# Kernel optimization log

Hardware: AMD Instinct MI355X
Metric: run time of the kernel (lower is better)

The kernel has to match this reference:

```python
import jax, jax.numpy as jnp
import numpy as np

NX = 768
N_HEAD = 12
R = 8
SCALING = 16.0  # lora_alpha*r / r = lora_alpha
NEG = 1e10


def setup_inputs() -> dict:
    key = jax.random.key(0)
    ks = jax.random.split(key, 7)
    B, S = 2, 2048
    return {
        "x": jax.random.normal(ks[0], (B, S, NX), dtype=jnp.float32),
        "w_attn": jax.random.normal(ks[1], (NX, 3 * NX), dtype=jnp.float32) * 0.02,
        "b_attn": jax.random.normal(ks[2], (3 * NX,), dtype=jnp.float32) * 0.02,
        "lora_A": jax.random.normal(ks[3], (3 * R, NX), dtype=jnp.float32) * 0.02,
        "lora_B": jax.random.normal(ks[4], (3 * NX, R), dtype=jnp.float32) * 0.02,
        "w_proj": jax.random.normal(ks[5], (NX, NX), dtype=jnp.float32) * 0.02,
        "b_proj": jax.random.normal(ks[6], (NX,), dtype=jnp.float32) * 0.02,
    }


def reference(x, w_attn, b_attn, lora_A, lora_B, w_proj, b_proj):
    B, S, _ = x.shape
    dh = NX // N_HEAD

    # --- LoRA-augmented QKV projection (MergedLinear, fan_in_fan_out=True, unmerged) ---
    qkv = x @ w_attn + b_attn  # [B,S,3*NX]
    A = lora_A.reshape(3, R, NX)          # per-chunk A_i: [r, nx]
    Bm = lora_B.reshape(3, NX, R)         # per-chunk B_i: [nx, r]
    # x @ (B_i @ A_i).T = (x @ A_i.T) @ B_i.T, grouped over q/k/v chunks c
    t = jnp.einsum('bsd,crd->bscr', x, A)           # [B,S,3,r]
    delta = jnp.einsum('bscr,cer->bsce', t, Bm)     # [B,S,3,nx]
    qkv = qkv + delta.reshape(B, S, 3 * NX) * SCALING

    # --- split heads ---
    q, k, v = jnp.split(qkv, 3, axis=-1)
    q = q.reshape(B, S, N_HEAD, dh).transpose(0, 2, 1, 3)  # [B,H,S,dh]
    k = k.reshape(B, S, N_HEAD, dh).transpose(0, 2, 1, 3)  # [B,H,S,dh]
    v = v.reshape(B, S, N_HEAD, dh).transpose(0, 2, 1, 3)  # [B,H,S,dh]

    # --- manual causal softmax attention (scale=True) ---
    w = jnp.einsum('bhqd,bhkd->bhqk', q, k) / jnp.sqrt(jnp.float32(dh))
    mask = jnp.tril(jnp.ones((S, S), dtype=w.dtype))[None, None]  # tril bias buffer
    w = w * mask - NEG * (1.0 - mask)
    w = jax.nn.softmax(w, axis=-1)
    a = jnp.einsum('bhqk,bhkd->bhqd', w, v)  # [B,H,S,dh]

    # --- merge heads + output projection (Conv1D) ---
    a = a.transpose(0, 2, 1, 3).reshape(B, S, NX)
    a = a @ w_proj + b_proj

    present = jnp.stack([k, v])  # [2,B,H,S,dh]
    return a, present
```

## Files before the change

### kernel.cpp

```cpp
#include <hip/hip_runtime.h>
#include <cstdint>

#define NXC 768
#define NHEAD 12
#define BB 2
#define SS 2048
#define MTOT (BB*SS)
#define NQKV (3*NXC)
#define PRESENT_HALF (BB*NHEAD*SS*64)

typedef __bf16 bf16x8 __attribute__((ext_vector_type(8)));
typedef float f32x4 __attribute__((ext_vector_type(4)));
typedef float f32x16 __attribute__((ext_vector_type(16)));

__device__ __forceinline__ uint16_t f2bf(float f) {
    uint32_t u = __builtin_bit_cast(uint32_t, f);
    uint32_t r = (u + 0x7FFFu + ((u >> 16) & 1u)) >> 16;
    return (uint16_t)r;
}

__device__ __forceinline__ bf16x8 vfrag(ushort4 a, ushort4 b) {
    union { bf16x8 v; ushort4 u[2]; } r;
    r.u[0] = a; r.u[1] = b;
    return r.v;
}

__device__ __forceinline__ void gload16(const uint16_t* g, uint16_t* l) {
    __builtin_amdgcn_global_load_lds(
        (const __attribute__((address_space(1))) unsigned int*)g,
        (__attribute__((address_space(3))) unsigned int*)l, 16, 0, 0);
}


__global__ __launch_bounds__(256) void prep_all(
    const float* __restrict__ x, uint16_t* __restrict__ x_bf,
    const float* __restrict__ w_attn, const float* __restrict__ lora_A,
    const float* __restrict__ lora_B, uint16_t* __restrict__ weffT,
    const float* __restrict__ w_proj, uint16_t* __restrict__ wpT) {
    __shared__ float T[64][65];
    __shared__ float Af[8][64];
    __shared__ float Bf[64][8];
    const int t = threadIdx.x;
    const int blk = blockIdx.x;
    if (blk < 3072) {
        int i = blk * 256 + t;
        float4 v = ((const float4*)x)[i];
        ushort4 o;
        o.x = f2bf(v.x); o.y = f2bf(v.y); o.z = f2bf(v.z); o.w = f2bf(v.w);
        ((ushort4*)x_bf)[i] = o;
        return;
    }
    if (blk < 3504) {
        const int i2 = blk - 3072;
        const int n0 = (i2 % 36) * 64, k0 = (i2 / 36) * 64;
        const int c = n0 / NXC;
        {
            const int nn = t & 63, q = t >> 6;
#pragma unroll
            for (int j = 0; j < 16; ++j) {
                int kr = q + j * 4;
                T[kr][nn] = w_attn[(size_t)(k0 + kr) * NQKV + n0 + nn];
            }
        }
        {
            int idx = t;
            Af[idx >> 6][idx & 63] = lora_A[(size_t)(c * 8 + (idx >> 6)) * NXC + k0 + (idx & 63)];
            idx += 256;
            Af[idx >> 6][idx & 63] = lora_A[(size_t)(c * 8 + (idx >> 6)) * NXC + k0 + (idx & 63)];
            Bf[t >> 3][t & 7] = lora_B[(size_t)(n0 + (t >> 3)) * 8 + (t & 7)];
            idx = t + 256;
            Bf[idx >> 3][idx & 7] = lora_B[(size_t)(n0 + (idx >> 3)) * 8 + (idx & 7)];
        }
        __syncthreads();
        const int kk = t & 63, q = t >> 6;
#pragma unroll
        for (int j = 0; j < 16; ++j) {
            int nn = q + j * 4;
            float d = 0.f;
#pragma unroll
            for (int r = 0; r < 8; ++r) d += Af[r][kk] * Bf[nn][r];
            weffT[(size_t)(n0 + nn) * NXC + k0 + kk] = f2bf(T[kk][nn] + 16.0f * d);
        }
        return;
    }
    {
        const int i3 = blk - 3504;
        const int n0 = (i3 % 12) * 64, k0 = (i3 / 12) * 64;
        {
            const int nn = t & 63, q = t >> 6;
#pragma unroll
            for (int j = 0; j < 16; ++j) {
                int kr = q + j * 4;
                T[kr][nn] = w_proj[(size_t)(k0 + kr) * NXC + n0 + nn];
            }
        }
        __syncthreads();
        const int kk = t & 63, q = t >> 6;
#pragma unroll
        for (int j = 0; j < 16; ++j) {
            int nn = q + j * 4;
            wpT[(size_t)(n0 + nn) * NXC + k0 + kk] = f2bf(T[kk][nn]);
        }
    }
}


template<int MODE, int BM, int BN, int NBX>
__global__ __launch_bounds__(256) void gemm_bt(
    const uint16_t* __restrict__ Abf, const uint16_t* __restrict__ BTbf,
    const float* __restrict__ bias, float* __restrict__ outf,
    uint16_t* __restrict__ q_bf, uint16_t* __restrict__ k_bf,
    uint16_t* __restrict__ vT_bf) {
    constexpr int MR = BM / 32;
    constexpr int NR = BN / 32;
    constexpr int AI = BM / 32;
    constexpr int BI = BN / 32;
    __shared__ uint16_t As[2][BM][64];
    __shared__ uint16_t Bs[2][BN][64];
    const int t = threadIdx.x;
    const int lane = t & 63;
    const int w = t >> 6;
    const int wr = (w >> 1) * (BM / 2);
    const int wc = (w & 1) * (BN / 2);
    const int lr16 = lane & 15;
    const int hi2 = lane >> 4;
    const int id = blockIdx.x;
    const int wgid = (id & 7) * ((int)gridDim.x >> 3) + (id >> 3);
    const int by = wgid / NBX, bx = wgid - by * NBX;
    const size_t arow0 = (size_t)by * BM;
    const size_t brow0 = (size_t)bx * BN;
    const int srow = lane >> 3;
    const int schunk = ((lane & 7) ^ (srow & 7)) << 3;
    const uint16_t* Asrc = Abf + (arow0 + w * (BM / 4) + srow) * NXC + schunk;
    const uint16_t* Bsrc = BTbf + (brow0 + w * (BN / 4) + srow) * NXC + schunk;

    f32x4 acc[MR][NR];
#pragma unroll
    for (int m = 0; m < MR; ++m)
#pragma unroll
        for (int n = 0; n < NR; ++n) acc[m][n] = (f32x4){0.f, 0.f, 0.f, 0.f};

#define STAGE(buf, k0) do { \
    _Pragma("unroll") \
    for (int j = 0; j < AI; ++j) \
        gload16(Asrc + (size_t)(j * 8) * NXC + (k0), &As[buf][w * (BM / 4) + j * 8][0]); \
    _Pragma("unroll") \
    for (int j = 0; j < BI; ++j) \
        gload16(Bsrc + (size_t)(j * 8) * NXC + (k0), &Bs[buf][w * (BN / 4) + j * 8][0]); \
} while (0)

    STAGE(0, 0);
    asm volatile("s_waitcnt vmcnt(0)" ::: "memory");
    __builtin_amdgcn_s_barrier();

    int cur = 0;
    for (int kt = 0; kt < 12; ++kt) {
        if (kt + 1 < 12) STAGE(cur ^ 1, (kt + 1) << 6);
        bf16x8 af[2][MR], bv[2][NR];
#pragma unroll
        for (int kk = 0; kk < 2; ++kk) {
#pragma unroll
            for (int m = 0; m < MR; ++m) {
                const int r = wr + m * 16 + lr16;
                af[kk][m] = *(const bf16x8*)&As[cur][r][(((kk * 4 + hi2) ^ (r & 7)) << 3)];
            }
#pragma unroll
            for (int n = 0; n < NR; ++n) {
                const int r = wc + n * 16 + lr16;
                bv[kk][n] = *(const bf16x8*)&Bs[cur][r][(((kk * 4 + hi2) ^ (r & 7)) << 3)];
            }
        }
        __builtin_amdgcn_s_setprio(1);
#pragma unroll
        for (int kk = 0; kk < 2; ++kk)
#pragma unroll
            for (int m = 0; m < MR; ++m)
#pragma unroll
                for (int n = 0; n < NR; ++n)
                    acc[m][n] = __builtin_amdgcn_mfma_f32_16x16x32_bf16(af[kk][m], bv[kk][n],
                                                                        acc[m][n], 0, 0, 0);
        __builtin_amdgcn_s_setprio(0);
        asm volatile("s_waitcnt vmcnt(0)" ::: "memory");
        __builtin_amdgcn_s_barrier();
        cur ^= 1;
    }
#undef STAGE

    const int rowb = (lane >> 4) << 2;
    const float QSCALE = 0.125f * 1.44269504f;
#pragma unroll
    for (int m = 0; m < MR; ++m) {
        int grow0 = (int)arow0 + wr + m * 16 + rowb;
#pragma unroll
        for (int n = 0; n < NR; ++n) {
            int gcol = (int)brow0 + wc + n * 16 + lr16;
            float bvs = bias[gcol];
            if (MODE == 1) {
#pragma unroll
                for (int ri = 0; ri < 4; ++ri) {
                    int grow = grow0 + ri;
                    outf[(size_t)grow * NXC + gcol] = acc[m][n][ri] + bvs;
                }
            } else {
                int c = gcol >= 2 * NXC ? 2 : (gcol >= NXC ? 1 : 0);
                int e = gcol - c * NXC;
                int h = e >> 6, d = e & 63;
                int b = grow0 >> 11, s0 = grow0 & 2047;
                if (c == 0) {
#pragma unroll
                    for (int ri = 0; ri < 4; ++ri) {
                        float v = acc[m][n][ri] + bvs;
                        q_bf[((size_t)(b * NHEAD + h) * SS + s0 + ri) * 64 + d] = f2bf(v * QSCALE);
                    }
                } else if (c == 1) {
#pragma unroll
                    for (int ri = 0; ri < 4; ++ri) {
                        float v = acc[m][n][ri] + bvs;
                        size_t hidx = (size_t)(b * NHEAD + h) * SS + s0 + ri;
                        k_bf[hidx * 64 + d] = f2bf(v);
                        outf[hidx * 64 + d] = v;
                    }
                } else {
                    float v0 = acc[m][n][0] + bvs, v1 = acc[m][n][1] + bvs;
                    float v2 = acc[m][n][2] + bvs, v3 = acc[m][n][3] + bvs;
                    ushort4 pv;
                    pv.x = f2bf(v0); pv.y = f2bf(v1); pv.z = f2bf(v2); pv.w = f2bf(v3);
                    *(ushort4*)(vT_bf + ((size_t)(b * NHEAD + h) * 64 + d) * SS + s0) = pv;
                    size_t hb = ((size_t)(b * NHEAD + h) * SS + s0) * 64 + d;
                    outf[PRESENT_HALF + hb] = v0;
                    outf[PRESENT_HALF + hb + 64] = v1;
                    outf[PRESENT_HALF + hb + 128] = v2;
                    outf[PRESENT_HALF + hb + 192] = v3;
                }
            }
        }
    }
}


__global__ __launch_bounds__(256) void attn_kernel(
    const uint16_t* __restrict__ qb, const uint16_t* __restrict__ kb,
    const uint16_t* __restrict__ vtb, uint16_t* __restrict__ ab) {
    __shared__ __align__(16) uint8_t smem[32768];
    uint16_t* KT0 = (uint16_t*)smem;
    uint16_t* VT0 = (uint16_t*)(smem + 16384);
    float* Mlp = (float*)smem;
    float* Llp = Mlp + 64;
    float* Ofp = Llp + 64;

    const int t = threadIdx.x;
    const int w = t >> 6, lane = t & 63;
    const int qw = w & 1, khalf = w >> 1;
    const int l31 = lane & 31, hi = lane >> 5;
    const int i8 = lane >> 3, c8 = lane & 7;
    const int id = blockIdx.x;
    const int xcd = id & 7, slot = id >> 3;
    const int lh = slot % 3, qs = slot / 3;
    const int qi = 31 - qs;
    const int bh = xcd * 3 + lh;
    const int qbase = qi * 64;
    const int q = qbase + qw * 32 + l31;
    const uint16_t* qh = qb + (size_t)bh * (SS * 64);
    const uint16_t* kh = kb + (size_t)bh * (SS * 64);
    const uint16_t* vh = vtb + (size_t)bh * (64 * SS);
    const int nkt = qi + 1;

    bf16x8 qf[4];
#pragma unroll
    for (int dc = 0; dc < 4; ++dc)
        qf[dc] = *(const bf16x8*)(qh + (size_t)q * 64 + dc * 16 + hi * 8);

    f32x16 o0, o1;
#pragma unroll
    for (int i = 0; i < 16; ++i) { o0[i] = 0.f; o1[i] = 0.f; }
    float m_run = -1e30f, l_run = 0.f;

    const uint16_t* ksrc = kh + (size_t)i8 * 64 + ((c8 ^ i8) << 3);
    const uint16_t* vsrc = vh + (size_t)i8 * SS + ((c8 ^ i8) << 3);
    const int j0 = (w & 1) * 4;

    if (khalf == 0) {
#pragma unroll
        for (int j = 0; j < 4; ++j)
            gload16(ksrc + (size_t)((j0 + j) * 8) * 64, KT0 + (j0 + j) * 8 * 64);
    } else {
#pragma unroll
        for (int j = 0; j < 4; ++j)
            gload16(vsrc + (size_t)((j0 + j) * 8) * SS, VT0 + (j0 + j) * 8 * 64);
    }
    asm volatile("s_waitcnt vmcnt(0)" ::: "memory");
    __syncthreads();

    int cur = 0;
    for (int kt = 0; kt < nkt; ++kt) {
        if (kt + 1 < nkt) {
            const int nb = (kt + 1) << 6;
            uint16_t* KTn = KT0 + (cur ^ 1) * 4096;
            uint16_t* VTn = VT0 + (cur ^ 1) * 4096;
            if (khalf == 0) {
#pragma unroll
                for (int j = 0; j < 4; ++j)
                    gload16(ksrc + (size_t)(nb + (j0 + j) * 8) * 64, KTn + (j0 + j) * 8 * 64);
            } else {
#pragma unroll
                for (int j = 0; j < 4; ++j)
                    gload16(vsrc + (size_t)((j0 + j) * 8) * SS + nb, VTn + (j0 + j) * 8 * 64);
            }
        }
        const uint16_t* KTc = KT0 + cur * 4096;
        const uint16_t* VTc = VT0 + cur * 4096;

        f32x16 sa;
#pragma unroll
        for (int i = 0; i < 16; ++i) sa[i] = 0.f;
        const int krow = khalf * 32 + l31;
        __builtin_amdgcn_s_setprio(1);
#pragma unroll
        for (int dc = 0; dc < 4; ++dc) {
            bf16x8 kf = *(const bf16x8*)(KTc + krow * 64 + (((dc * 2 + hi) ^ (l31 & 7)) << 3));
            sa = __builtin_amdgcn_mfma_f32_32x32x16_bf16(kf, qf[dc], sa, 0, 0, 0);
        }
        __builtin_amdgcn_s_setprio(0);
        if (kt == qi) {
            const int qrel = qw * 32 + l31;
#pragma unroll
            for (int r = 0; r < 16; ++r) {
                int key = khalf * 32 + (r & 3) + 8 * (r >> 2) + 4 * hi;
                sa[r] = (key > qrel) ? -1e30f : sa[r];
            }
        }
        float m8[8];
#pragma unroll
        for (int g = 0; g < 8; ++g) m8[g] = fmaxf(sa[g * 2], sa[g * 2 + 1]);
        float lm = fmaxf(fmaxf(fmaxf(m8[0], m8[1]), fmaxf(m8[2], m8[3])),
                         fmaxf(fmaxf(m8[4], m8[5]), fmaxf(m8[6], m8[7])));
        if (__any(lm > m_run + 8.f)) {
            float tmf = fmaxf(lm, __shfl_xor(lm, 32));
            float nm = fmaxf(m_run, tmf);
            float corr = __builtin_amdgcn_exp2f(m_run - nm);
            l_run *= corr;
#pragma unroll
            for (int i = 0; i < 16; ++i) { o0[i] *= corr; o1[i] *= corr; }
            m_run = nm;
        }
        float e[16];
#pragma unroll
        for (int r = 0; r < 16; ++r) e[r] = __builtin_amdgcn_exp2f(sa[r] - m_run);
        bf16x8 pa0, pa1;
#pragma unroll
        for (int r = 0; r < 8; ++r) { pa0[r] = (__bf16)e[r]; pa1[r] = (__bf16)e[8 + r]; }
        l_run += ((e[0] + e[1]) + (e[2] + e[3])) + ((e[4] + e[5]) + (e[6] + e[7]))
               + ((e[8] + e[9]) + (e[10] + e[11])) + ((e[12] + e[13]) + (e[14] + e[15]));
        const int rx = l31 & 7;
        __builtin_amdgcn_s_setprio(1);
#pragma unroll
        for (int dblk = 0; dblk < 2; ++dblk) {
            const uint16_t* vrow = VTc + (dblk * 32 + l31) * 64;
            ushort4 v0 = *(const ushort4*)(vrow + (((khalf * 4 + 0) ^ rx) << 3) + hi * 4);
            ushort4 v1 = *(const ushort4*)(vrow + (((khalf * 4 + 1) ^ rx) << 3) + hi * 4);
            ushort4 v2 = *(const ushort4*)(vrow + (((khalf * 4 + 2) ^ rx) << 3) + hi * 4);
            ushort4 v3 = *(const ushort4*)(vrow + (((khalf * 4 + 3) ^ rx) << 3) + hi * 4);
            f32x16 oo = dblk ? o1 : o0;
            oo = __builtin_amdgcn_mfma_f32_32x32x16_bf16(vfrag(v0, v1), pa0, oo, 0, 0, 0);
            oo = __builtin_amdgcn_mfma_f32_32x32x16_bf16(vfrag(v2, v3), pa1, oo, 0, 0, 0);
            if (dblk) o1 = oo; else o0 = oo;
        }
        __builtin_amdgcn_s_setprio(0);
        asm volatile("s_waitcnt vmcnt(0)" ::: "memory");
        __syncthreads();
        cur ^= 1;
    }

    const float lf = l_run + __shfl_xor(l_run, 32);
    const int qrow = qw * 32 + l31;
    if (khalf == 1) {
        if (hi == 0) { Mlp[qrow] = m_run; Llp[qrow] = lf; }
#pragma unroll
        for (int dblk = 0; dblk < 2; ++dblk)
#pragma unroll
            for (int rg = 0; rg < 4; ++rg) {
                f32x16 oo = dblk ? o1 : o0;
                f32x4 v;
                v[0] = oo[rg * 4 + 0]; v[1] = oo[rg * 4 + 1];
                v[2] = oo[rg * 4 + 2]; v[3] = oo[rg * 4 + 3];
                *(f32x4*)&Ofp[qrow * 68 + dblk * 32 + rg * 8 + hi * 4] = v;
            }
    }
    __syncthreads();
    if (khalf == 0) {
        const float m2 = Mlp[qrow], l2 = Llp[qrow];
        const float ms = fmaxf(m_run, m2);
        const float wA = __builtin_amdgcn_exp2f(m_run - ms);
        const float wB = __builtin_amdgcn_exp2f(m2 - ms);
        const float inv = 1.f / (lf * wA + l2 * wB);
        const int b = bh / NHEAD, h = bh - b * NHEAD;
        uint16_t* abp = ab + ((size_t)(b * SS + q)) * NXC + h * 64;
#pragma unroll
        for (int dblk = 0; dblk < 2; ++dblk)
#pragma unroll
            for (int rg = 0; rg < 4; ++rg) {
                f32x16 oo = dblk ? o1 : o0;
                f32x4 po = *(const f32x4*)&Ofp[qrow * 68 + dblk * 32 + rg * 8 + hi * 4];
                ushort4 wv;
                wv.x = f2bf((oo[rg * 4 + 0] * wA + po[0] * wB) * inv);
                wv.y = f2bf((oo[rg * 4 + 1] * wA + po[1] * wB) * inv);
                wv.z = f2bf((oo[rg * 4 + 2] * wA + po[2] * wB) * inv);
                wv.w = f2bf((oo[rg * 4 + 3] * wA + po[3] * wB) * inv);
                *(ushort4*)(abp + dblk * 32 + rg * 8 + hi * 4) = wv;
            }
    }
}


extern "C" void kernel_launch(void* const* d_in, const int* in_sizes, int n_in,
                              void* d_out, int out_size, void* d_ws, size_t ws_size,
                              hipStream_t stream) {
    const float* x      = (const float*)d_in[0];
    const float* w_attn = (const float*)d_in[1];
    const float* b_attn = (const float*)d_in[2];
    const float* lora_A = (const float*)d_in[3];
    const float* lora_B = (const float*)d_in[4];
    const float* w_proj = (const float*)d_in[5];
    const float* b_proj = (const float*)d_in[6];
    float* out = (float*)d_out;
    float* present = out + (size_t)MTOT * NXC;

    uint16_t* ws    = (uint16_t*)d_ws;
    uint16_t* x_bf  = ws;
    uint16_t* weffT = x_bf + 3145728;
    uint16_t* wpT   = weffT + 1769472;
    uint16_t* q_bf  = wpT + 589824;
    uint16_t* k_bf  = q_bf + 3145728;
    uint16_t* vT_bf = k_bf + 3145728;
    uint16_t* a_bf  = vT_bf + 3145728;

    prep_all<<<dim3(3648), dim3(256), 0, stream>>>(x, x_bf, w_attn, lora_A, lora_B,
                                                   weffT, w_proj, wpT);
    gemm_bt<0, 128, 64, 36><<<dim3(1152), dim3(256), 0, stream>>>(
        x_bf, weffT, b_attn, present, q_bf, k_bf, vT_bf);
    attn_kernel<<<dim3(768), dim3(256), 0, stream>>>(q_bf, k_bf, vT_bf, a_bf);
    gemm_bt<1, 128, 64, 12><<<dim3(384), dim3(256), 0, stream>>>(
        a_bf, wpT, b_proj, out, nullptr, nullptr, nullptr);
}
```

Measured before the change: 89.59 us.

## Triple-buffer K/V tiles in attention with partial vmcnt waits

Moves the attention kernel's K/V staging from double to triple buffering in LDS (48KB). Loads run two tiles ahead, and the kernel waits only for the older batch (vmcnt(4)) before a single barrier per iteration, replacing the full drain and sync at the end of each iteration. This aims to hide global-load latency behind the MFMA work. The larger LDS footprint may lower occupancy, and correctness depends on the barrier placement protecting the buffer being overwritten.

```diff
diff --git a/kernel.cpp b/kernel.cpp
--- a/kernel.cpp
+++ b/kernel.cpp
@@ -241,9 +241,9 @@
 __global__ __launch_bounds__(256) void attn_kernel(
     const uint16_t* __restrict__ qb, const uint16_t* __restrict__ kb,
     const uint16_t* __restrict__ vtb, uint16_t* __restrict__ ab) {
-    __shared__ __align__(16) uint8_t smem[32768];
+    __shared__ __align__(16) uint8_t smem[49152];
     uint16_t* KT0 = (uint16_t*)smem;
-    uint16_t* VT0 = (uint16_t*)(smem + 16384);
+    uint16_t* VT0 = (uint16_t*)(smem + 24576);
     float* Mlp = (float*)smem;
     float* Llp = Mlp + 64;
     float* Ofp = Llp + 64;
@@ -279,33 +279,32 @@
     const uint16_t* vsrc = vh + (size_t)i8 * SS + ((c8 ^ i8) << 3);
     const int j0 = (w & 1) * 4;
 
-    if (khalf == 0) {
-#pragma unroll
-        for (int j = 0; j < 4; ++j)
-            gload16(ksrc + (size_t)((j0 + j) * 8) * 64, KT0 + (j0 + j) * 8 * 64);
-    } else {
-#pragma unroll
-        for (int j = 0; j < 4; ++j)
-            gload16(vsrc + (size_t)((j0 + j) * 8) * SS, VT0 + (j0 + j) * 8 * 64);
-    }
-    asm volatile("s_waitcnt vmcnt(0)" ::: "memory");
-    __syncthreads();
+#define ASTAGE(buf, nb) do { \
+    if (khalf == 0) { \
+        uint16_t* KTn = KT0 + (buf) * 4096; \
+        _Pragma("unroll") \
+        for (int j = 0; j < 4; ++j) \
+            gload16(ksrc + (size_t)((nb) + (j0 + j) * 8) * 64, KTn + (j0 + j) * 8 * 64); \
+    } else { \
+        uint16_t* VTn = VT0 + (buf) * 4096; \
+        _Pragma("unroll") \
+        for (int j = 0; j < 4; ++j) \
+            gload16(vsrc + (size_t)((j0 + j) * 8) * SS + (nb), VTn + (j0 + j) * 8 * 64); \
+    } \
+} while (0)
+
+    ASTAGE(0, 0);
+    if (nkt > 1) ASTAGE(1, 64);
 
     int cur = 0;
     for (int kt = 0; kt < nkt; ++kt) {
-        if (kt + 1 < nkt) {
-            const int nb = (kt + 1) << 6;
-            uint16_t* KTn = KT0 + (cur ^ 1) * 4096;
-            uint16_t* VTn = VT0 + (cur ^ 1) * 4096;
-            if (khalf == 0) {
-#pragma unroll
-                for (int j = 0; j < 4; ++j)
-                    gload16(ksrc + (size_t)(nb + (j0 + j) * 8) * 64, KTn + (j0 + j) * 8 * 64);
-            } else {
-#pragma unroll
-                for (int j = 0; j < 4; ++j)
-                    gload16(vsrc + (size_t)((j0 + j) * 8) * SS + nb, VTn + (j0 + j) * 8 * 64);
-            }
+        if (kt + 1 < nkt) asm volatile("s_waitcnt vmcnt(4)" ::: "memory");
+        else              asm volatile("s_waitcnt vmcnt(0)" ::: "memory");
+        __builtin_amdgcn_s_barrier();
+        __builtin_amdgcn_sched_barrier(0);
+        if (kt + 2 < nkt) {
+            int b2 = cur + 2; if (b2 >= 3) b2 -= 3;
+            ASTAGE(b2, (kt + 2) << 6);
         }
         const uint16_t* KTc = KT0 + cur * 4096;
         const uint16_t* VTc = VT0 + cur * 4096;
@@ -366,10 +365,11 @@
             if (dblk) o1 = oo; else o0 = oo;
         }
         __builtin_amdgcn_s_setprio(0);
-        asm volatile("s_waitcnt vmcnt(0)" ::: "memory");
-        __syncthreads();
-        cur ^= 1;
-    }
+        cur = (cur == 2) ? 0 : cur + 1;
+    }
+#undef ASTAGE
+
+    __syncthreads();
 
     const float lf = l_run + __shfl_xor(l_run, 32);
     const int qrow = qw * 32 + l31;
```

Measured after the change: 89.41 us. No clear change (-0.2%).
